# Kernel tuning notes

Measured on AMD Instinct MI355X. Metric: run time of the kernel, lower is better.

## Reference

```python
import jax, jax.numpy as jnp
import numpy as np

B, S, E = 2, 2048, 2048
H, HKV, D = 16, 8, 64          # num_heads, num_kv_heads, head_dim = E//H//2
NREP = H // HKV
DEPTH = 12
LAMBDA_INIT = 0.8 - 0.6 * float(np.exp(-0.3 * DEPTH))
EPS = 1e-5
SCALE = D ** -0.5
NEG = -1e30


def setup_inputs() -> dict:
    key = jax.random.key(0)
    ks = jax.random.split(key, 10)
    x = jax.random.normal(ks[0], (B, S, E), jnp.float32)
    # rotary tables (seq_len, head_dim/2)
    inv_freq = 1.0 / (10000.0 ** (np.arange(0, D, 2, dtype=np.float32) / D))
    freqs = jnp.asarray(np.outer(np.arange(S, dtype=np.float32), inv_freq), jnp.float32)
    cos, sin = jnp.cos(freqs), jnp.sin(freqs)
    Wq = jax.random.normal(ks[1], (E, E), jnp.float32) * 0.02
    Wk = jax.random.normal(ks[2], (E // NREP, E), jnp.float32) * 0.02
    Wv = jax.random.normal(ks[3], (E // NREP, E), jnp.float32) * 0.02
    Wo = jax.random.normal(ks[4], (E, E), jnp.float32) * 0.02
    lambda_q1 = jax.random.normal(ks[5], (D,), jnp.float32) * 0.1
    lambda_k1 = jax.random.normal(ks[6], (D,), jnp.float32) * 0.1
    lambda_q2 = jax.random.normal(ks[7], (D,), jnp.float32) * 0.1
    lambda_k2 = jax.random.normal(ks[8], (D,), jnp.float32) * 0.1
    subln_w = jnp.ones((2 * D,), jnp.float32)
    return dict(x=x, cos=cos, sin=sin, Wq=Wq, Wk=Wk, Wv=Wv, Wo=Wo,
                lambda_q1=lambda_q1, lambda_k1=lambda_k1,
                lambda_q2=lambda_q2, lambda_k2=lambda_k2, subln_w=subln_w)


def _rotary_interleaved(x, cos, sin):
    # x: (B, S, nh, D); cos/sin: (S, D//2); interleaved pairs (even, odd)
    x1, x2 = x[..., 0::2], x[..., 1::2]
    c = cos[None, :, None, :]
    s = sin[None, :, None, :]
    o1 = x1 * c - x2 * s
    o2 = x1 * s + x2 * c
    return jnp.stack([o1, o2], axis=-1).reshape(x.shape)


def _causal_attn(qh, kh, vcat, mask):
    # qh: (B,S,H,D); kh: (B,S,HKV,D); vcat: (B,S,HKV,2D)
    kr = jnp.repeat(kh, NREP, axis=2)      # GQA repeat -> (B,S,H,D)
    vr = jnp.repeat(vcat, NREP, axis=2)    # (B,S,H,2D)
    scores = jnp.einsum('bqhd,bkhd->bhqk', qh, kr) * SCALE
    scores = jnp.where(mask, scores, NEG)
    p = jax.nn.softmax(scores, axis=-1)
    return jnp.einsum('bhqk,bkhd->bqhd', p, vr)  # (B,S,H,2D)


def reference(x, cos, sin, Wq, Wk, Wv, Wo, lambda_q1, lambda_k1, lambda_q2, lambda_k2, subln_w):
    q = (x @ Wq.T).reshape(B, S, 2 * H, D)
    k = (x @ Wk.T).reshape(B, S, 2 * HKV, D)
    v = (x @ Wv.T).reshape(B, S, HKV, 2, D)
    q = _rotary_interleaved(q, cos, sin).reshape(B, S, H, 2, D)
    k = _rotary_interleaved(k, cos, sin).reshape(B, S, HKV, 2, D)
    vcat = v.reshape(B, S, HKV, 2 * D)  # concat(v1, v2) along last dim
    mask = jnp.tril(jnp.ones((S, S), bool))[None, None]
    a1 = _causal_attn(q[..., 0, :], k[..., 0, :], vcat, mask)
    a2 = _causal_attn(q[..., 1, :], k[..., 1, :], vcat, mask)
    lam = (jnp.exp(jnp.sum(lambda_q1 * lambda_k1))
           - jnp.exp(jnp.sum(lambda_q2 * lambda_k2)) + LAMBDA_INIT)
    a = a1 - lam * a2                      # (B,S,H,2D)
    # RMSNorm over last dim with affine weight, then fixed (1 - lambda_init) scale
    a = a * jax.lax.rsqrt(jnp.mean(a * a, axis=-1, keepdims=True) + EPS) * subln_w
    a = a * (1.0 - LAMBDA_INIT)
    return a.reshape(B, S, E) @ Wo.T
```

## Files before the change

### kernel.cpp

```cpp
#include <hip/hip_runtime.h>

#define LAMBDA_INIT 0.78360576653162448f

typedef __attribute__((ext_vector_type(8))) short short8;
typedef __attribute__((ext_vector_type(4))) float f32x4;

__device__ __forceinline__ unsigned short f2bf(float f) {
  unsigned int u; __builtin_memcpy(&u, &f, 4);
  u += 0x7fffu + ((u >> 16) & 1u);
  return (unsigned short)(u >> 16);
}
__device__ __forceinline__ short8 cvt8(float4 a, float4 b) {
  short8 s;
  s[0] = (short)f2bf(a.x); s[1] = (short)f2bf(a.y);
  s[2] = (short)f2bf(a.z); s[3] = (short)f2bf(a.w);
  s[4] = (short)f2bf(b.x); s[5] = (short)f2bf(b.y);
  s[6] = (short)f2bf(b.z); s[7] = (short)f2bf(b.w);
  return s;
}

#define GLOAD_LDS16(g, l)                                                     \
  __builtin_amdgcn_global_load_lds(                                           \
      (const __attribute__((address_space(1))) void*)(g),                     \
      (__attribute__((address_space(3))) void*)(l), 16, 0, 0)

__global__ void conv_bf16(const float* __restrict__ in,
                          unsigned short* __restrict__ outp, int n8) {
  const int i = blockIdx.x * 256 + threadIdx.x;
  if (i >= n8) return;
  const float4 a = *(const float4*)(in + (size_t)i * 8);
  const float4 b = *(const float4*)(in + (size_t)i * 8 + 4);
  *(short8*)(outp + (size_t)i * 8) = cvt8(a, b);
}

__global__ void conv_all(const float* __restrict__ x, const float* __restrict__ wq,
                         const float* __restrict__ wk, const float* __restrict__ wv,
                         const float* __restrict__ wo, unsigned short* __restrict__ ws) {
  const int i = blockIdx.x * 256 + threadIdx.x;
  const float* src; size_t so; unsigned short* dst;
  if (i < 1048576)      { src = x;  so = i;           dst = ws; }
  else if (i < 1572864) { src = wq; so = i - 1048576; dst = ws + 8388608; }
  else if (i < 1835008) { src = wk; so = i - 1572864; dst = ws + 12582912; }
  else if (i < 2097152) { src = wv; so = i - 1835008; dst = ws + 14680064; }
  else                  { src = wo; so = i - 2097152; dst = ws + 16777216; }
  const float4 a = *(const float4*)(src + so * 8);
  const float4 b = *(const float4*)(src + so * 8 + 4);
  *(short8*)(dst + so * 8) = cvt8(a, b);
}


__global__ __launch_bounds__(256, 2)
void qkv_bb(const unsigned short* __restrict__ xb,
            const unsigned short* __restrict__ Wqb, const unsigned short* __restrict__ Wkb,
            const unsigned short* __restrict__ Wvb, const float* __restrict__ cosb,
            const float* __restrict__ sinb,
            unsigned short* __restrict__ Qb, unsigned short* __restrict__ Kb,
            unsigned short* __restrict__ Vtb) {
  __shared__ __align__(16) unsigned short As[128 * 64];
  __shared__ __align__(16) unsigned short Bs[128 * 64];
  const int t = threadIdx.x;
  const int wave = t >> 6, lane = t & 63;
  const int l15 = lane & 15, l4 = lane >> 4;
  const int wm = (wave >> 1) * 64, wn = (wave & 1) * 64;
  const int m0 = blockIdx.y * 128, n0 = blockIdx.x * 128;
  const int crow = t >> 3, ccol = (t & 7) * 8;
  const unsigned short* Ag = xb + (size_t)m0 * 2048;

  const unsigned short* Bgh; int ntype;
  if (n0 < 2048)      { Bgh = Wqb + (size_t)n0 * 2048;          ntype = 0; }
  else if (n0 < 3072) { Bgh = Wkb + (size_t)(n0 - 2048) * 2048; ntype = 1; }
  else                { Bgh = Wvb + (size_t)(n0 - 3072) * 2048; ntype = 2; }

  const f32x4 fzero = {0.f, 0.f, 0.f, 0.f};
  f32x4 acc[4][4];
#pragma unroll
  for (int i = 0; i < 4; i++)
#pragma unroll
    for (int j = 0; j < 4; j++) acc[i][j] = fzero;

  for (int kt = 0; kt < 32; ++kt) {
    const int k0 = kt << 6;
    __syncthreads();
#pragma unroll
    for (int j = 0; j < 4; j++) {
      GLOAD_LDS16(Ag + (size_t)(j * 32 + crow) * 2048 + k0 + ccol,
                  &As[j * 2048 + wave * 512]);
      GLOAD_LDS16(Bgh + (size_t)(j * 32 + crow) * 2048 + k0 + ccol,
                  &Bs[j * 2048 + wave * 512]);
    }
    __syncthreads();
#pragma unroll
    for (int ks = 0; ks < 2; ++ks) {
      short8 af[4], bfr[4];
#pragma unroll
      for (int mi = 0; mi < 4; mi++)
        af[mi] = *(const short8*)(&As[(wm + mi * 16 + l15) * 64 + ks * 32 + l4 * 8]);
#pragma unroll
      for (int ni = 0; ni < 4; ni++)
        bfr[ni] = *(const short8*)(&Bs[(wn + ni * 16 + l15) * 64 + ks * 32 + l4 * 8]);
#pragma unroll
      for (int mi = 0; mi < 4; mi++)
#pragma unroll
        for (int ni = 0; ni < 4; ni++)
          acc[mi][ni] = __builtin_amdgcn_mfma_f32_16x16x32_bf16(af[mi], bfr[ni], acc[mi][ni], 0, 0, 0);
    }
  }
#pragma unroll
  for (int mi = 0; mi < 4; mi++)
#pragma unroll
    for (int ni = 0; ni < 4; ni++)
#pragma unroll
      for (int r = 0; r < 4; r++) {
        const int m = m0 + wm + mi * 16 + l4 * 4 + r;
        const int n = n0 + wn + ni * 16 + l15;
        float fv = acc[mi][ni][r];
        if (ntype < 2) {
          const int s = m & 2047;
          const int j = (n & 63) >> 1;
          const float c = cosb[s * 32 + j];
          const float sn = sinb[s * 32 + j];
          const float p = __shfl_xor(fv, 1);
          fv = (n & 1) ? (p * sn + fv * c) : (fv * c - p * sn);
        }
        if (ntype == 0)
          Qb[(size_t)m * 2048 + n] = f2bf(fv);
        else if (ntype == 1)
          Kb[(size_t)m * 1024 + (n - 2048)] = f2bf(fv);
        else
          Vtb[((size_t)((m >> 11) * 1024 + (n - 3072))) * 2048 + (m & 2047)] = f2bf(fv);
      }
}

__global__ __launch_bounds__(256, 2)
void o_bb(const unsigned short* __restrict__ Ab, const unsigned short* __restrict__ Wob,
          float* __restrict__ C) {
  __shared__ __align__(16) unsigned short As[128 * 64];
  __shared__ __align__(16) unsigned short Bs[128 * 64];
  const int t = threadIdx.x;
  const int wave = t >> 6, lane = t & 63;
  const int l15 = lane & 15, l4 = lane >> 4;
  const int wm = (wave >> 1) * 64, wn = (wave & 1) * 64;
  const int m0 = blockIdx.y * 128, n0 = blockIdx.x * 128;
  const int crow = t >> 3, ccol = (t & 7) * 8;
  const unsigned short* Ag = Ab + (size_t)m0 * 2048;
  const unsigned short* Bgh = Wob + (size_t)n0 * 2048;

  const f32x4 fzero = {0.f, 0.f, 0.f, 0.f};
  f32x4 acc[4][4];
#pragma unroll
  for (int i = 0; i < 4; i++)
#pragma unroll
    for (int j = 0; j < 4; j++) acc[i][j] = fzero;

  for (int kt = 0; kt < 32; ++kt) {
    const int k0 = kt << 6;
    __syncthreads();
#pragma unroll
    for (int j = 0; j < 4; j++) {
      GLOAD_LDS16(Ag + (size_t)(j * 32 + crow) * 2048 + k0 + ccol,
                  &As[j * 2048 + wave * 512]);
      GLOAD_LDS16(Bgh + (size_t)(j * 32 + crow) * 2048 + k0 + ccol,
                  &Bs[j * 2048 + wave * 512]);
    }
    __syncthreads();
#pragma unroll
    for (int ks = 0; ks < 2; ++ks) {
      short8 af[4], bfr[4];
#pragma unroll
      for (int mi = 0; mi < 4; mi++)
        af[mi] = *(const short8*)(&As[(wm + mi * 16 + l15) * 64 + ks * 32 + l4 * 8]);
#pragma unroll
      for (int ni = 0; ni < 4; ni++)
        bfr[ni] = *(const short8*)(&Bs[(wn + ni * 16 + l15) * 64 + ks * 32 + l4 * 8]);
#pragma unroll
      for (int mi = 0; mi < 4; mi++)
#pragma unroll
        for (int ni = 0; ni < 4; ni++)
          acc[mi][ni] = __builtin_amdgcn_mfma_f32_16x16x32_bf16(af[mi], bfr[ni], acc[mi][ni], 0, 0, 0);
    }
  }
#pragma unroll
  for (int mi = 0; mi < 4; mi++)
#pragma unroll
    for (int ni = 0; ni < 4; ni++)
#pragma unroll
      for (int r = 0; r < 4; r++) {
        const int m = m0 + wm + mi * 16 + l4 * 4 + r;
        const int n = n0 + wn + ni * 16 + l15;
        C[(size_t)m * 2048 + n] = acc[mi][ni][r];
      }
}


__global__ __launch_bounds__(256, 2)
void qkv_gemm_f32(const unsigned short* __restrict__ xb,
                  const float* __restrict__ Wq, const float* __restrict__ Wk,
                  const float* __restrict__ Wv, const float* __restrict__ cosb,
                  const float* __restrict__ sinb,
                  unsigned short* __restrict__ Qb, unsigned short* __restrict__ Kb,
                  unsigned short* __restrict__ Vtb) {
  __shared__ __align__(16) unsigned short As[128 * 64];
  __shared__ __align__(16) unsigned short Bs[128 * 72];
  const int t = threadIdx.x;
  const int wave = t >> 6, lane = t & 63;
  const int l15 = lane & 15, l4 = lane >> 4;
  const int wm = (wave >> 1) * 64, wn = (wave & 1) * 64;
  const int m0 = blockIdx.y * 128, n0 = blockIdx.x * 128;
  const int crow = t >> 3, ccol = (t & 7) * 8;
  const unsigned short* Ag = xb + (size_t)m0 * 2048;

  const float* Bg; int ntype;
  if (n0 < 2048)      { Bg = Wq + (size_t)n0 * 2048;          ntype = 0; }
  else if (n0 < 3072) { Bg = Wk + (size_t)(n0 - 2048) * 2048; ntype = 1; }
  else                { Bg = Wv + (size_t)(n0 - 3072) * 2048; ntype = 2; }

  const f32x4 fzero = {0.f, 0.f, 0.f, 0.f};
  f32x4 acc[4][4];
#pragma unroll
  for (int i = 0; i < 4; i++)
#pragma unroll
    for (int j = 0; j < 4; j++) acc[i][j] = fzero;

  float4 rbf[4][2];
#pragma unroll
  for (int i = 0; i < 4; i++) {
    rbf[i][0] = *(const float4*)(Bg + (size_t)(crow + 32 * i) * 2048 + ccol);
    rbf[i][1] = *(const float4*)(Bg + (size_t)(crow + 32 * i) * 2048 + ccol + 4);
  }
  for (int kt = 0; kt < 32; ++kt) {
    const int k0 = kt << 6;
    __syncthreads();
#pragma unroll
    for (int j = 0; j < 4; j++)
      GLOAD_LDS16(Ag + (size_t)(j * 32 + crow) * 2048 + k0 + ccol,
                  &As[j * 2048 + wave * 512]);
#pragma unroll
    for (int i = 0; i < 4; i++)
      *(short8*)(&Bs[(crow + 32 * i) * 72 + ccol]) = cvt8(rbf[i][0], rbf[i][1]);
    __syncthreads();
    if (kt + 1 < 32) {
      const int kn = k0 + 64;
#pragma unroll
      for (int i = 0; i < 4; i++) {
        rbf[i][0] = *(const float4*)(Bg + (size_t)(crow + 32 * i) * 2048 + kn + ccol);
        rbf[i][1] = *(const float4*)(Bg + (size_t)(crow + 32 * i) * 2048 + kn + ccol + 4);
      }
    }
#pragma unroll
    for (int ks = 0; ks < 2; ++ks) {
      short8 af[4], bfr[4];
#pragma unroll
      for (int mi = 0; mi < 4; mi++)
        af[mi] = *(const short8*)(&As[(wm + mi * 16 + l15) * 64 + ks * 32 + l4 * 8]);
#pragma unroll
      for (int ni = 0; ni < 4; ni++)
        bfr[ni] = *(const short8*)(&Bs[(wn + ni * 16 + l15) * 72 + ks * 32 + l4 * 8]);
#pragma unroll
      for (int mi = 0; mi < 4; mi++)
#pragma unroll
        for (int ni = 0; ni < 4; ni++)
          acc[mi][ni] = __builtin_amdgcn_mfma_f32_16x16x32_bf16(af[mi], bfr[ni], acc[mi][ni], 0, 0, 0);
    }
  }
#pragma unroll
  for (int mi = 0; mi < 4; mi++)
#pragma unroll
    for (int ni = 0; ni < 4; ni++)
#pragma unroll
      for (int r = 0; r < 4; r++) {
        const int m = m0 + wm + mi * 16 + l4 * 4 + r;
        const int n = n0 + wn + ni * 16 + l15;
        float fv = acc[mi][ni][r];
        if (ntype < 2) {
          const int s = m & 2047;
          const int j = (n & 63) >> 1;
          const float c = cosb[s * 32 + j];
          const float sn = sinb[s * 32 + j];
          const float p = __shfl_xor(fv, 1);
          fv = (n & 1) ? (p * sn + fv * c) : (fv * c - p * sn);
        }
        if (ntype == 0)
          Qb[(size_t)m * 2048 + n] = f2bf(fv);
        else if (ntype == 1)
          Kb[(size_t)m * 1024 + (n - 2048)] = f2bf(fv);
        else
          Vtb[((size_t)((m >> 11) * 1024 + (n - 3072))) * 2048 + (m & 2047)] = f2bf(fv);
      }
}

__global__ __launch_bounds__(256, 2)
void o_gemm_f32(const unsigned short* __restrict__ Ab, const float* __restrict__ Wo,
                float* __restrict__ C) {
  __shared__ __align__(16) unsigned short As[128 * 64];
  __shared__ __align__(16) unsigned short Bs[128 * 72];
  const int t = threadIdx.x;
  const int wave = t >> 6, lane = t & 63;
  const int l15 = lane & 15, l4 = lane >> 4;
  const int wm = (wave >> 1) * 64, wn = (wave & 1) * 64;
  const int m0 = blockIdx.y * 128, n0 = blockIdx.x * 128;
  const int crow = t >> 3, ccol = (t & 7) * 8;
  const unsigned short* Ag = Ab + (size_t)m0 * 2048;
  const float* Bg = Wo + (size_t)n0 * 2048;

  const f32x4 fzero = {0.f, 0.f, 0.f, 0.f};
  f32x4 acc[4][4];
#pragma unroll
  for (int i = 0; i < 4; i++)
#pragma unroll
    for (int j = 0; j < 4; j++) acc[i][j] = fzero;

  float4 rbf[4][2];
#pragma unroll
  for (int i = 0; i < 4; i++) {
    rbf[i][0] = *(const float4*)(Bg + (size_t)(crow + 32 * i) * 2048 + ccol);
    rbf[i][1] = *(const float4*)(Bg + (size_t)(crow + 32 * i) * 2048 + ccol + 4);
  }
  for (int kt = 0; kt < 32; ++kt) {
    const int k0 = kt << 6;
    __syncthreads();
#pragma unroll
    for (int j = 0; j < 4; j++)
      GLOAD_LDS16(Ag + (size_t)(j * 32 + crow) * 2048 + k0 + ccol,
                  &As[j * 2048 + wave * 512]);
#pragma unroll
    for (int i = 0; i < 4; i++)
      *(short8*)(&Bs[(crow + 32 * i) * 72 + ccol]) = cvt8(rbf[i][0], rbf[i][1]);
    __syncthreads();
    if (kt + 1 < 32) {
      const int kn = k0 + 64;
#pragma unroll
      for (int i = 0; i < 4; i++) {
        rbf[i][0] = *(const float4*)(Bg + (size_t)(crow + 32 * i) * 2048 + kn + ccol);
        rbf[i][1] = *(const float4*)(Bg + (size_t)(crow + 32 * i) * 2048 + kn + ccol + 4);
      }
    }
#pragma unroll
    for (int ks = 0; ks < 2; ++ks) {
      short8 af[4], bfr[4];
#pragma unroll
      for (int mi = 0; mi < 4; mi++)
        af[mi] = *(const short8*)(&As[(wm + mi * 16 + l15) * 64 + ks * 32 + l4 * 8]);
#pragma unroll
      for (int ni = 0; ni < 4; ni++)
        bfr[ni] = *(const short8*)(&Bs[(wn + ni * 16 + l15) * 72 + ks * 32 + l4 * 8]);
#pragma unroll
      for (int mi = 0; mi < 4; mi++)
#pragma unroll
        for (int ni = 0; ni < 4; ni++)
          acc[mi][ni] = __builtin_amdgcn_mfma_f32_16x16x32_bf16(af[mi], bfr[ni], acc[mi][ni], 0, 0, 0);
    }
  }
#pragma unroll
  for (int mi = 0; mi < 4; mi++)
#pragma unroll
    for (int ni = 0; ni < 4; ni++)
#pragma unroll
      for (int r = 0; r < 4; r++) {
        const int m = m0 + wm + mi * 16 + l4 * 4 + r;
        const int n = n0 + wn + ni * 16 + l15;
        C[(size_t)m * 2048 + n] = acc[mi][ni][r];
      }
}

__global__ __launch_bounds__(128, 2)
void attn_kernel(const unsigned short* __restrict__ Q,
                 const unsigned short* __restrict__ Kb,
                 const unsigned short* __restrict__ Vt,
                 unsigned short* __restrict__ Ab,
                 const float* __restrict__ lq1,
                 const float* __restrict__ lk1,
                 const float* __restrict__ lq2,
                 const float* __restrict__ lk2,
                 const float* __restrict__ wsub) {
  const int pi = blockIdx.x;
  const int bh = blockIdx.y;
  const int b = bh >> 4, h = bh & 15, hk = h >> 1;

  __shared__ __align__(16) unsigned short Ks[2][2][64 * 64];
  __shared__ __align__(16) unsigned short Vs[2][128 * 64];
  __shared__ __align__(16) unsigned short Ps[64 * 64];

  const int t = threadIdx.x;
  const int wave = t >> 6, lane = t & 63;
  const int l15 = lane & 15, l4 = lane >> 4;
  const int crow = t >> 3, ccol = (t & 7) * 8;
  const int swc = ccol ^ ((crow & 7) << 3);

  float s1 = 0.f, s2 = 0.f;
  for (int i = 0; i < 64; i++) {
    s1 += lq1[i] * lk1[i];
    s2 += lq2[i] * lk2[i];
  }
  const float lam = __expf(s1) - __expf(s2) + LAMBDA_INIT;

  float wv[8];
#pragma unroll
  for (int nt = 0; nt < 8; nt++) wv[nt] = wsub[nt * 16 + l15];

  short8 onesf;
#pragma unroll
  for (int j = 0; j < 8; j++) onesf[j] = (l15 == 0) ? (short)0x3F80 : (short)0;

  const f32x4 fzero = {0.f, 0.f, 0.f, 0.f};
  const unsigned short* Kgb = Kb + ((size_t)(b * 2048)) * 1024 + 2 * hk * 64;
  const unsigned short* Vgb = Vt + ((size_t)((b * 8 + hk) * 128)) * 2048;

#define STAGE_KV(KT, BUF)                                                     \
  do {                                                                        \
    const int k0s = (KT) << 6;                                                \
    _Pragma("unroll")                                                         \
    for (int c_ = 0; c_ < 2; c_++)                                            \
      _Pragma("unroll")                                                       \
      for (int i_ = 0; i_ < 4; i_++)                                          \
        GLOAD_LDS16(Kgb + (size_t)(k0s + i_ * 16 + crow) * 1024 + c_ * 64 + swc, \
                    &Ks[BUF][c_][i_ * 1024 + wave * 512]);                    \
    _Pragma("unroll")                                                         \
    for (int i_ = 0; i_ < 8; i_++)                                            \
      GLOAD_LDS16(Vgb + (size_t)(i_ * 16 + crow) * 2048 + k0s + swc,          \
                  &Vs[BUF][i_ * 1024 + wave * 512]);                          \
  } while (0)

  for (int half = 0; half < 2; ++half) {
    const int qi = half ? (31 - pi) : pi;
    const int q0 = qi * 64;
    const int nkt = qi + 1;

    short8 qf[2][2][2];
#pragma unroll
    for (int s = 0; s < 2; s++)
#pragma unroll
      for (int c = 0; c < 2; c++)
#pragma unroll
        for (int ks = 0; ks < 2; ks++)
          qf[s][c][ks] = *(const short8*)(Q + ((size_t)(b * 2048 + q0 + wave * 32 + s * 16 + l15)) * 2048
                                            + (2 * h + c) * 64 + ks * 32 + l4 * 8);

    f32x4 accO[2][2][8];
    f32x4 accL[2][2];
#pragma unroll
    for (int s = 0; s < 2; s++)
#pragma unroll
      for (int c = 0; c < 2; c++) {
        accL[s][c] = fzero;
#pragma unroll
        for (int nt = 0; nt < 8; nt++) accO[s][c][nt] = fzero;
      }

    __syncthreads();
    STAGE_KV(0, 0);

    for (int kt = 0; kt < nkt; ++kt) {
      const int k0 = kt << 6;
      const int cur = kt & 1;
      __syncthreads();
      if (kt + 1 < nkt) STAGE_KV(kt + 1, cur ^ 1);

      const unsigned short* Ksb0 = &Ks[cur][0][0];
      const unsigned short* Ksb1 = &Ks[cur][1][0];
      const unsigned short* Vsb  = &Vs[cur][0];

      short8 pf[2][2][2];
#pragma unroll
      for (int c = 0; c < 2; c++) {
        const unsigned short* Ksb = c ? Ksb1 : Ksb0;
#pragma unroll
        for (int ct = 0; ct < 4; ct++) {
          const int kr = ct * 16 + l15;
          const int ksw = (kr & 7) << 3;
          const short8 kb0 = *(const short8*)(&Ksb[kr * 64 + ((l4 * 8) ^ ksw)]);
          const short8 kb1 = *(const short8*)(&Ksb[kr * 64 + ((32 + l4 * 8) ^ ksw)]);
#pragma unroll
          for (int s = 0; s < 2; s++) {
            f32x4 z = fzero;
            z = __builtin_amdgcn_mfma_f32_16x16x32_bf16(qf[s][c][0], kb0, z, 0, 0, 0);
            z = __builtin_amdgcn_mfma_f32_16x16x32_bf16(qf[s][c][1], kb1, z, 0, 0, 0);
            const int rbase = wave * 32 + s * 16 + l4 * 4;
            const bool needm = (k0 + 63) > (q0 + wave * 32 + s * 16);
#pragma unroll
            for (int r = 0; r < 4; r++) {
              float e = exp2f(fmaf(z[r], 0.18033688011112042f, -23.083120654223414f));
              if (needm && (k0 + ct * 16 + l15) > (q0 + rbase + r)) e = 0.f;
              const int prow = rbase + r;
              Ps[prow * 64 + ((ct * 16 + l15) ^ ((prow & 7) << 3))] = f2bf(e);
            }
          }
        }
#pragma unroll
        for (int s = 0; s < 2; s++) {
          const int prow = wave * 32 + s * 16 + l15;
          const int psw = (l15 & 7) << 3;
#pragma unroll
          for (int ks = 0; ks < 2; ks++)
            pf[s][c][ks] = *(const short8*)(&Ps[prow * 64 + ((ks * 32 + l4 * 8) ^ psw)]);
        }
      }

      __builtin_amdgcn_s_setprio(1);
#pragma unroll
      for (int nt = 0; nt < 8; nt++) {
        const int vrow = nt * 16 + l15;
        const int vsw = (vrow & 7) << 3;
        const short8 v0 = *(const short8*)(&Vsb[vrow * 64 + ((l4 * 8) ^ vsw)]);
        const short8 v1 = *(const short8*)(&Vsb[vrow * 64 + ((32 + l4 * 8) ^ vsw)]);
#pragma unroll
        for (int s = 0; s < 2; s++) {
          accO[s][0][nt] = __builtin_amdgcn_mfma_f32_16x16x32_bf16(pf[s][0][0], v0, accO[s][0][nt], 0, 0, 0);
          accO[s][0][nt] = __builtin_amdgcn_mfma_f32_16x16x32_bf16(pf[s][0][1], v1, accO[s][0][nt], 0, 0, 0);
          accO[s][1][nt] = __builtin_amdgcn_mfma_f32_16x16x32_bf16(pf[s][1][0], v0, accO[s][1][nt], 0, 0, 0);
          accO[s][1][nt] = __builtin_amdgcn_mfma_f32_16x16x32_bf16(pf[s][1][1], v1, accO[s][1][nt], 0, 0, 0);
        }
      }
#pragma unroll
      for (int s = 0; s < 2; s++)
#pragma unroll
        for (int c = 0; c < 2; c++) {
          accL[s][c] = __builtin_amdgcn_mfma_f32_16x16x32_bf16(pf[s][c][0], onesf, accL[s][c], 0, 0, 0);
          accL[s][c] = __builtin_amdgcn_mfma_f32_16x16x32_bf16(pf[s][c][1], onesf, accL[s][c], 0, 0, 0);
        }
      __builtin_amdgcn_s_setprio(0);
    }

#pragma unroll
    for (int s = 0; s < 2; s++)
#pragma unroll
      for (int r = 0; r < 4; r++) {
        const float l1 = __shfl(accL[s][0][r], lane & 48);
        const float l2 = __shfl(accL[s][1][r], lane & 48);
        const float i1 = 1.f / fmaxf(l1, 1e-30f);
        const float i2 = lam / fmaxf(l2, 1e-30f);
        float av[8], ss = 0.f;
#pragma unroll
        for (int nt = 0; nt < 8; nt++) {
          const float a = accO[s][0][nt][r] * i1 - accO[s][1][nt][r] * i2;
          av[nt] = a;
          ss += a * a;
        }
#pragma unroll
        for (int off = 1; off < 16; off <<= 1) ss += __shfl_xor(ss, off, 16);
        const float sca = rsqrtf(ss * (1.f / 128.f) + 1e-5f) * (1.f - LAMBDA_INIT);
        const int qrow = q0 + wave * 32 + s * 16 + l4 * 4 + r;
        unsigned short* Ao = Ab + ((size_t)(b * 2048 + qrow)) * 2048 + h * 128;
#pragma unroll
        for (int nt = 0; nt < 8; nt++)
          Ao[nt * 16 + l15] = f2bf(av[nt] * sca * wv[nt]);
      }
  }
#undef STAGE_KV
}

extern "C" void kernel_launch(void* const* d_in, const int* in_sizes, int n_in,
                              void* d_out, int out_size, void* d_ws, size_t ws_size,
                              hipStream_t stream) {
  const float* x    = (const float*)d_in[0];
  const float* cosb = (const float*)d_in[1];
  const float* sinb = (const float*)d_in[2];
  const float* Wq   = (const float*)d_in[3];
  const float* Wk   = (const float*)d_in[4];
  const float* Wv   = (const float*)d_in[5];
  const float* Wo   = (const float*)d_in[6];
  const float* lq1  = (const float*)d_in[7];
  const float* lk1  = (const float*)d_in[8];
  const float* lq2  = (const float*)d_in[9];
  const float* lk2  = (const float*)d_in[10];
  const float* wsub = (const float*)d_in[11];
  float* out = (float*)d_out;

  unsigned short* XA  = (unsigned short*)d_ws;
  unsigned short* Kb  = (unsigned short*)d_out;
  unsigned short* Vtb = Kb + (size_t)4096 * 1024;
  unsigned short* Qb  = Vtb + (size_t)2 * 1024 * 2048;

  dim3 blk(256);
  dim3 ablk(128);
  if (ws_size >= (size_t)41943040) {
    unsigned short* Wqb = XA + 8388608;
    unsigned short* Wkb = XA + 12582912;
    unsigned short* Wvb = XA + 14680064;
    unsigned short* Wob = XA + 16777216;
    conv_all<<<10240, blk, 0, stream>>>(x, Wq, Wk, Wv, Wo, XA);
    qkv_bb<<<dim3(32, 32), blk, 0, stream>>>(XA, Wqb, Wkb, Wvb, cosb, sinb, Qb, Kb, Vtb);
    attn_kernel<<<dim3(16, 32), ablk, 0, stream>>>(Qb, Kb, Vtb, XA, lq1, lk1, lq2, lk2, wsub);
    o_bb<<<dim3(16, 32), blk, 0, stream>>>(XA, Wob, out);
  } else {
    conv_bf16<<<4096, blk, 0, stream>>>(x, XA, 1048576);
    qkv_gemm_f32<<<dim3(32, 32), blk, 0, stream>>>(XA, Wq, Wk, Wv, cosb, sinb, Qb, Kb, Vtb);
    attn_kernel<<<dim3(16, 32), ablk, 0, stream>>>(Qb, Kb, Vtb, XA, lq1, lk1, lq2, lk2, wsub);
    o_gemm_f32<<<dim3(16, 32), blk, 0, stream>>>(XA, Wo, out);
  }
}
```

Before: 432.8 us.

## Split attention block across four waves with 16 query rows each

The attention kernel now launches 256 threads (4 waves) per block instead of 128 (2 waves). Each wave handles 16 query rows rather than 32, and the K/V staging loops are halved because twice as many threads share the loads. This cuts per-wave register use (accumulators and Q fragments are halved) and adds waves to hide MFMA and exp latency. In exchange, K/V fragments read from LDS are reused across fewer MFMAs per wave, so LDS read traffic per unit of work goes up.

```diff
diff --git a/kernel.cpp b/kernel.cpp
--- a/kernel.cpp
+++ b/kernel.cpp
@@ -362,7 +362,7 @@
       }
 }
 
-__global__ __launch_bounds__(128, 2)
+__global__ __launch_bounds__(256, 2)
 void attn_kernel(const unsigned short* __restrict__ Q,
                  const unsigned short* __restrict__ Kb,
                  const unsigned short* __restrict__ Vt,
@@ -411,13 +411,13 @@
     _Pragma("unroll")                                                         \
     for (int c_ = 0; c_ < 2; c_++)                                            \
       _Pragma("unroll")                                                       \
-      for (int i_ = 0; i_ < 4; i_++)                                          \
-        GLOAD_LDS16(Kgb + (size_t)(k0s + i_ * 16 + crow) * 1024 + c_ * 64 + swc, \
-                    &Ks[BUF][c_][i_ * 1024 + wave * 512]);                    \
+      for (int i_ = 0; i_ < 2; i_++)                                          \
+        GLOAD_LDS16(Kgb + (size_t)(k0s + i_ * 32 + crow) * 1024 + c_ * 64 + swc, \
+                    &Ks[BUF][c_][i_ * 2048 + wave * 512]);                    \
     _Pragma("unroll")                                                         \
-    for (int i_ = 0; i_ < 8; i_++)                                            \
-      GLOAD_LDS16(Vgb + (size_t)(i_ * 16 + crow) * 2048 + k0s + swc,          \
-                  &Vs[BUF][i_ * 1024 + wave * 512]);                          \
+    for (int i_ = 0; i_ < 4; i_++)                                            \
+      GLOAD_LDS16(Vgb + (size_t)(i_ * 32 + crow) * 2048 + k0s + swc,          \
+                  &Vs[BUF][i_ * 2048 + wave * 512]);                          \
   } while (0)
 
   for (int half = 0; half < 2; ++half) {
@@ -425,26 +425,22 @@
     const int q0 = qi * 64;
     const int nkt = qi + 1;
 
-    short8 qf[2][2][2];
-#pragma unroll
-    for (int s = 0; s < 2; s++)
-#pragma unroll
-      for (int c = 0; c < 2; c++)
-#pragma unroll
-        for (int ks = 0; ks < 2; ks++)
-          qf[s][c][ks] = *(const short8*)(Q + ((size_t)(b * 2048 + q0 + wave * 32 + s * 16 + l15)) * 2048
-                                            + (2 * h + c) * 64 + ks * 32 + l4 * 8);
-
-    f32x4 accO[2][2][8];
-    f32x4 accL[2][2];
-#pragma unroll
-    for (int s = 0; s < 2; s++)
-#pragma unroll
-      for (int c = 0; c < 2; c++) {
-        accL[s][c] = fzero;
-#pragma unroll
-        for (int nt = 0; nt < 8; nt++) accO[s][c][nt] = fzero;
-      }
+    short8 qf[2][2];
+#pragma unroll
+    for (int c = 0; c < 2; c++)
+#pragma unroll
+      for (int ks = 0; ks < 2; ks++)
+        qf[c][ks] = *(const short8*)(Q + ((size_t)(b * 2048 + q0 + wave * 16 + l15)) * 2048
+                                       + (2 * h + c) * 64 + ks * 32 + l4 * 8);
+
+    f32x4 accO[2][8];
+    f32x4 accL[2];
+#pragma unroll
+    for (int c = 0; c < 2; c++) {
+      accL[c] = fzero;
+#pragma unroll
+      for (int nt = 0; nt < 8; nt++) accO[c][nt] = fzero;
+    }
 
     __syncthreads();
     STAGE_KV(0, 0);
@@ -459,7 +455,7 @@
       const unsigned short* Ksb1 = &Ks[cur][1][0];
       const unsigned short* Vsb  = &Vs[cur][0];
 
-      short8 pf[2][2][2];
+      short8 pf[2][2];
 #pragma unroll
       for (int c = 0; c < 2; c++) {
         const unsigned short* Ksb = c ? Ksb1 : Ksb0;
@@ -469,29 +465,25 @@
           const int ksw = (kr & 7) << 3;
           const short8 kb0 = *(const short8*)(&Ksb[kr * 64 + ((l4 * 8) ^ ksw)]);
           const short8 kb1 = *(const short8*)(&Ksb[kr * 64 + ((32 + l4 * 8) ^ ksw)]);
-#pragma unroll
-          for (int s = 0; s < 2; s++) {
-            f32x4 z = fzero;
-            z = __builtin_amdgcn_mfma_f32_16x16x32_bf16(qf[s][c][0], kb0, z, 0, 0, 0);
-            z = __builtin_amdgcn_mfma_f32_16x16x32_bf16(qf[s][c][1], kb1, z, 0, 0, 0);
-            const int rbase = wave * 32 + s * 16 + l4 * 4;
-            const bool needm = (k0 + 63) > (q0 + wave * 32 + s * 16);
-#pragma unroll
-            for (int r = 0; r < 4; r++) {
-              float e = exp2f(fmaf(z[r], 0.18033688011112042f, -23.083120654223414f));
-              if (needm && (k0 + ct * 16 + l15) > (q0 + rbase + r)) e = 0.f;
-              const int prow = rbase + r;
-              Ps[prow * 64 + ((ct * 16 + l15) ^ ((prow & 7) << 3))] = f2bf(e);
-            }
+          f32x4 z = fzero;
+          z = __builtin_amdgcn_mfma_f32_16x16x32_bf16(qf[c][0], kb0, z, 0, 0, 0);
+          z = __builtin_amdgcn_mfma_f32_16x16x32_bf16(qf[c][1], kb1, z, 0, 0, 0);
+          const int rbase = wave * 16 + l4 * 4;
+          const bool needm = (k0 + 63) > (q0 + wave * 16);
+#pragma unroll
+          for (int r = 0; r < 4; r++) {
+            float e = exp2f(fmaf(z[r], 0.18033688011112042f, -23.083120654223414f));
+            if (needm && (k0 + ct * 16 + l15) > (q0 + rbase + r)) e = 0.f;
+            const int prow = rbase + r;
+            Ps[prow * 64 + ((ct * 16 + l15) ^ ((prow & 7) << 3))] = f2bf(e);
           }
         }
-#pragma unroll
-        for (int s = 0; s < 2; s++) {
-          const int prow = wave * 32 + s * 16 + l15;
+        {
+          const int prow = wave * 16 + l15;
           const int psw = (l15 & 7) << 3;
 #pragma unroll
           for (int ks = 0; ks < 2; ks++)
-            pf[s][c][ks] = *(const short8*)(&Ps[prow * 64 + ((ks * 32 + l4 * 8) ^ psw)]);
+            pf[c][ks] = *(const short8*)(&Ps[prow * 64 + ((ks * 32 + l4 * 8) ^ psw)]);
         }
       }
 
@@ -502,48 +494,41 @@
         const int vsw = (vrow & 7) << 3;
         const short8 v0 = *(const short8*)(&Vsb[vrow * 64 + ((l4 * 8) ^ vsw)]);
         const short8 v1 = *(const short8*)(&Vsb[vrow * 64 + ((32 + l4 * 8) ^ vsw)]);
-#pragma unroll
-        for (int s = 0; s < 2; s++) {
-          accO[s][0][nt] = __builtin_amdgcn_mfma_f32_16x16x32_bf16(pf[s][0][0], v0, accO[s][0][nt], 0, 0, 0);
-          accO[s][0][nt] = __builtin_amdgcn_mfma_f32_16x16x32_bf16(pf[s][0][1], v1, accO[s][0][nt], 0, 0, 0);
-          accO[s][1][nt] = __builtin_amdgcn_mfma_f32_16x16x32_bf16(pf[s][1][0], v0, accO[s][1][nt], 0, 0, 0);
-          accO[s][1][nt] = __builtin_amdgcn_mfma_f32_16x16x32_bf16(pf[s][1][1], v1, accO[s][1][nt], 0, 0, 0);
-        }
-      }
-#pragma unroll
-      for (int s = 0; s < 2; s++)
-#pragma unroll
-        for (int c = 0; c < 2; c++) {
-          accL[s][c] = __builtin_amdgcn_mfma_f32_16x16x32_bf16(pf[s][c][0], onesf, accL[s][c], 0, 0, 0);
-          accL[s][c] = __builtin_amdgcn_mfma_f32_16x16x32_bf16(pf[s][c][1], onesf, accL[s][c], 0, 0, 0);
-        }
+        accO[0][nt] = __builtin_amdgcn_mfma_f32_16x16x32_bf16(pf[0][0], v0, accO[0][nt], 0, 0, 0);
+        accO[0][nt] = __builtin_amdgcn_mfma_f32_16x16x32_bf16(pf[0][1], v1, accO[0][nt], 0, 0, 0);
+        accO[1][nt] = __builtin_amdgcn_mfma_f32_16x16x32_bf16(pf[1][0], v0, accO[1][nt], 0, 0, 0);
+        accO[1][nt] = __builtin_amdgcn_mfma_f32_16x16x32_bf16(pf[1][1], v1, accO[1][nt], 0, 0, 0);
+      }
+#pragma unroll
+      for (int c = 0; c < 2; c++) {
+        accL[c] = __builtin_amdgcn_mfma_f32_16x16x32_bf16(pf[c][0], onesf, accL[c], 0, 0, 0);
+        accL[c] = __builtin_amdgcn_mfma_f32_16x16x32_bf16(pf[c][1], onesf, accL[c], 0, 0, 0);
+      }
       __builtin_amdgcn_s_setprio(0);
     }
 
 #pragma unroll
-    for (int s = 0; s < 2; s++)
-#pragma unroll
-      for (int r = 0; r < 4; r++) {
-        const float l1 = __shfl(accL[s][0][r], lane & 48);
-        const float l2 = __shfl(accL[s][1][r], lane & 48);
-        const float i1 = 1.f / fmaxf(l1, 1e-30f);
-        const float i2 = lam / fmaxf(l2, 1e-30f);
-        float av[8], ss = 0.f;
-#pragma unroll
-        for (int nt = 0; nt < 8; nt++) {
-          const float a = accO[s][0][nt][r] * i1 - accO[s][1][nt][r] * i2;
-          av[nt] = a;
-          ss += a * a;
-        }
-#pragma unroll
-        for (int off = 1; off < 16; off <<= 1) ss += __shfl_xor(ss, off, 16);
-        const float sca = rsqrtf(ss * (1.f / 128.f) + 1e-5f) * (1.f - LAMBDA_INIT);
-        const int qrow = q0 + wave * 32 + s * 16 + l4 * 4 + r;
-        unsigned short* Ao = Ab + ((size_t)(b * 2048 + qrow)) * 2048 + h * 128;
-#pragma unroll
-        for (int nt = 0; nt < 8; nt++)
-          Ao[nt * 16 + l15] = f2bf(av[nt] * sca * wv[nt]);
-      }
+    for (int r = 0; r < 4; r++) {
+      const float l1 = __shfl(accL[0][r], lane & 48);
+      const float l2 = __shfl(accL[1][r], lane & 48);
+      const float i1 = 1.f / fmaxf(l1, 1e-30f);
+      const float i2 = lam / fmaxf(l2, 1e-30f);
+      float av[8], ss = 0.f;
+#pragma unroll
+      for (int nt = 0; nt < 8; nt++) {
+        const float a = accO[0][nt][r] * i1 - accO[1][nt][r] * i2;
+        av[nt] = a;
+        ss += a * a;
+      }
+#pragma unroll
+      for (int off = 1; off < 16; off <<= 1) ss += __shfl_xor(ss, off, 16);
+      const float sca = rsqrtf(ss * (1.f / 128.f) + 1e-5f) * (1.f - LAMBDA_INIT);
+      const int qrow = q0 + wave * 16 + l4 * 4 + r;
+      unsigned short* Ao = Ab + ((size_t)(b * 2048 + qrow)) * 2048 + h * 128;
+#pragma unroll
+      for (int nt = 0; nt < 8; nt++)
+        Ao[nt * 16 + l15] = f2bf(av[nt] * sca * wv[nt]);
+    }
   }
 #undef STAGE_KV
 }
@@ -571,7 +556,6 @@
   unsigned short* Qb  = Vtb + (size_t)2 * 1024 * 2048;
 
   dim3 blk(256);
-  dim3 ablk(128);
   if (ws_size >= (size_t)41943040) {
     unsigned short* Wqb = XA + 8388608;
     unsigned short* Wkb = XA + 12582912;
@@ -579,12 +563,12 @@
     unsigned short* Wob = XA + 16777216;
     conv_all<<<10240, blk, 0, stream>>>(x, Wq, Wk, Wv, Wo, XA);
     qkv_bb<<<dim3(32, 32), blk, 0, stream>>>(XA, Wqb, Wkb, Wvb, cosb, sinb, Qb, Kb, Vtb);
-    attn_kernel<<<dim3(16, 32), ablk, 0, stream>>>(Qb, Kb, Vtb, XA, lq1, lk1, lq2, lk2, wsub);
+    attn_kernel<<<dim3(16, 32), blk, 0, stream>>>(Qb, Kb, Vtb, XA, lq1, lk1, lq2, lk2, wsub);
     o_bb<<<dim3(16, 32), blk, 0, stream>>>(XA, Wob, out);
   } else {
     conv_bf16<<<4096, blk, 0, stream>>>(x, XA, 1048576);
     qkv_gemm_f32<<<dim3(32, 32), blk, 0, stream>>>(XA, Wq, Wk, Wv, cosb, sinb, Qb, Kb, Vtb);
-    attn_kernel<<<dim3(16, 32), ablk, 0, stream>>>(Qb, Kb, Vtb, XA, lq1, lk1, lq2, lk2, wsub);
+    attn_kernel<<<dim3(16, 32), blk, 0, stream>>>(Qb, Kb, Vtb, XA, lq1, lk1, lq2, lk2, wsub);
     o_gemm_f32<<<dim3(16, 32), blk, 0, stream>>>(XA, Wo, out);
   }
 }
```

Result: faster. 384.9 us (-11.1%).
